# Optimization experiments

Measured on AMD Instinct MI355X. Metric: run time of the kernel, lower is better.

## Reference

```python
import jax, jax.numpy as jnp
import numpy as np
import math

B, T = 2, 1024
D, H, L = 1024, 16, 2
DH = D // H          # 64
R = DH // 2          # 32 rotation blocks
AV, OV = 1024, 16384
FF = 4 * D


def _ln(x, g, b, eps=1e-5):
    m = jnp.mean(x, axis=-1, keepdims=True)
    v = jnp.var(x, axis=-1, keepdims=True)
    return (x - m) * jax.lax.rsqrt(v + eps) * g + b


def build_block_diag_rotations(delta):
    # delta: (B,T,R) angles -> (B,T,2R,2R) block-diagonal 2x2 rotations
    c, s = jnp.cos(delta), jnp.sin(delta)
    Bd, Td, Rd = delta.shape
    M = jnp.zeros((Bd, Td, 2 * Rd, 2 * Rd), dtype=delta.dtype)
    i = 2 * jnp.arange(Rd)
    M = M.at[..., i, i].set(c)
    M = M.at[..., i + 1, i + 1].set(c)
    M = M.at[..., i, i + 1].set(-s)
    M = M.at[..., i + 1, i].set(s)
    return M


def parallel_prefix_product(M):
    # cumulative matrix product along seq axis (associative scan)
    return jax.lax.associative_scan(jnp.matmul, M, axis=1)


def setup_inputs() -> dict:
    key = jax.random.key(0)
    ks = jax.random.split(key, 32)
    std = 0.02
    p = {
        "actions": jax.random.randint(ks[0], (B, T), 0, AV),
        "observations": jax.random.randint(ks[1], (B, T), 0, OV),
        "action_emb": jax.random.normal(ks[2], (AV, D), jnp.float32) * std,
        "obs_emb": jax.random.normal(ks[3], (OV, D), jnp.float32) * std,
        "lie_w": jax.random.normal(ks[4], (D, R), jnp.float32) * std,
        "lie_b": jnp.zeros((R,), jnp.float32),
        "Wq": jax.random.normal(ks[5], (L, D, D), jnp.float32) * std,
        "bq": jnp.zeros((L, D), jnp.float32),
        "Wk": jax.random.normal(ks[6], (L, D, D), jnp.float32) * std,
        "bk": jnp.zeros((L, D), jnp.float32),
        "Wv": jax.random.normal(ks[7], (L, D, D), jnp.float32) * std,
        "bv": jnp.zeros((L, D), jnp.float32),
        "Wo": jax.random.normal(ks[8], (L, D, D), jnp.float32) * std,
        "bo": jnp.zeros((L, D), jnp.float32),
        "ln1_g": jnp.ones((L, D), jnp.float32),
        "ln1_b": jnp.zeros((L, D), jnp.float32),
        "ln2_g": jnp.ones((L, D), jnp.float32),
        "ln2_b": jnp.zeros((L, D), jnp.float32),
        "w1": jax.random.normal(ks[9], (L, D, FF), jnp.float32) * std,
        "b1": jnp.zeros((L, FF), jnp.float32),
        "w2": jax.random.normal(ks[10], (L, FF, D), jnp.float32) * std,
        "b2": jnp.zeros((L, D), jnp.float32),
        "out_g": jnp.ones((D,), jnp.float32),
        "out_bln": jnp.zeros((D,), jnp.float32),
        "out_w": jax.random.normal(ks[11], (D, OV), jnp.float32) * std,
        "out_b": jnp.zeros((OV,), jnp.float32),
    }
    return p


def reference(actions, observations, action_emb, obs_emb, lie_w, lie_b,
              Wq, bq, Wk, bk, Wv, bv, Wo, bo,
              ln1_g, ln1_b, ln2_g, ln2_b, w1, b1, w2, b2,
              out_g, out_bln, out_w, out_b):
    # position state: action embeddings -> Lie algebra -> SO(d_head) prefix products
    a_emb = action_emb[actions]                      # (B,T,D)
    delta = a_emb @ lie_w + lie_b                    # (B,T,R)
    M = build_block_diag_rotations(delta)            # (B,T,DH,DH)
    P = parallel_prefix_product(M)                   # (B,T,DH,DH)

    x = obs_emb[observations]                        # (B,T,D)
    causal = jnp.triu(jnp.ones((T, T), dtype=bool), k=1)
    scale = math.sqrt(DH)

    for l in range(L):
        h = _ln(x, ln1_g[l], ln1_b[l])
        Q = (h @ Wq[l] + bq[l]).reshape(B, T, H, DH)
        K = (h @ Wk[l] + bk[l]).reshape(B, T, H, DH)
        V = (h @ Wv[l] + bv[l]).reshape(B, T, H, DH)
        # generalized RoPE: rotate every head by the cumulative matrix P_t
        Qr = jnp.einsum('btij,bthj->bthi', P, Q)
        Kr = jnp.einsum('btij,bthj->bthi', P, K)
        scores = jnp.einsum('bthd,bshd->bhts', Qr, Kr) / scale
        scores = jnp.where(causal, -jnp.inf, scores)
        attn = jax.nn.softmax(scores, axis=-1)
        o = jnp.einsum('bhts,bshd->bthd', attn, V).reshape(B, T, D)
        x = x + (o @ Wo[l] + bo[l])
        h2 = _ln(x, ln2_g[l], ln2_b[l])
        x = x + (jax.nn.gelu(h2 @ w1[l] + b1[l], approximate=False) @ w2[l] + b2[l])

    x = _ln(x, out_g, out_bln)
    return x @ out_w + out_b                         # (B,T,OV)
```

## Files before the change

### kernel.cpp

```cpp
#include <hip/hip_runtime.h>
#include <cstdint>
#include <cstddef>


using u16 = unsigned short;
using u32 = unsigned int;

typedef __bf16 bf16x8 __attribute__((ext_vector_type(8)));
typedef float  f32x4  __attribute__((ext_vector_type(4)));

__device__ __forceinline__ u16 f2bf(float f) {
  union { float f; u32 u; } v; v.f = f;
  u32 r = v.u + 0x7fffu + ((v.u >> 16) & 1u);
  return (u16)(r >> 16);
}
__device__ __forceinline__ float bf2f(u16 u) {
  union { u32 u; float f; } v; v.u = ((u32)u) << 16;
  return v.f;
}

__device__ __forceinline__ void gll16(const void* g, void* l) {
  __builtin_amdgcn_global_load_lds((__attribute__((address_space(1))) void*)(g),
                                   (__attribute__((address_space(3))) void*)(l),
                                   16, 0, 0);
}

__global__ __launch_bounds__(256) void transpose_f2b(
    const float* __restrict__ in, u16* __restrict__ out, int K, int N)
{
  __shared__ float tile[64][65];
  const int n0 = blockIdx.x * 64, k0 = blockIdx.y * 64;
  const int tid = threadIdx.x;
  const int rr = tid >> 4, cc = (tid & 15) * 4;
  #pragma unroll
  for (int p = 0; p < 4; ++p) {
    int kk = rr + p * 16;
    float4 v = *(const float4*)(in + (size_t)(k0 + kk) * N + n0 + cc);
    tile[kk][cc] = v.x; tile[kk][cc + 1] = v.y;
    tile[kk][cc + 2] = v.z; tile[kk][cc + 3] = v.w;
  }
  __syncthreads();
  #pragma unroll
  for (int p = 0; p < 4; ++p) {
    int nn = rr + p * 16;
    u32 lo = (u32)f2bf(tile[cc + 0][nn]) | ((u32)f2bf(tile[cc + 1][nn]) << 16);
    u32 hi = (u32)f2bf(tile[cc + 2][nn]) | ((u32)f2bf(tile[cc + 3][nn]) << 16);
    uint2 pk; pk.x = lo; pk.y = hi;
    *(uint2*)(out + (size_t)(n0 + nn) * K + k0 + cc) = pk;
  }
}

__global__ __launch_bounds__(256) void fuse_bias(
    const float* __restrict__ bq, const float* __restrict__ bk,
    const float* __restrict__ bv, float* __restrict__ out)
{
  int idx = blockIdx.x * 256 + threadIdx.x;
  int l = idx / 3072, r = idx % 3072;
  const float* src = (r < 1024) ? bq : ((r < 2048) ? bk : bv);
  out[idx] = src[l * 1024 + (r & 1023)];
}

__global__ __launch_bounds__(256) void delta_kernel(
    const int* __restrict__ actions, const float* __restrict__ aemb,
    const float* __restrict__ lie_w, const float* __restrict__ lie_b,
    float* __restrict__ delta)
{
  const int bt = blockIdx.x;
  const int a = actions[bt];
  const float* e = aemb + (size_t)a * 1024;
  const int r = threadIdx.x >> 3, part = threadIdx.x & 7;
  float s = 0.f;
  const int j0 = part * 128;
  for (int j = j0; j < j0 + 128; ++j)
    s += e[j] * lie_w[(size_t)j * 32 + r];
  s += __shfl_xor(s, 1); s += __shfl_xor(s, 2); s += __shfl_xor(s, 4);
  if (part == 0) delta[(size_t)bt * 32 + r] = s + lie_b[r];
}

__global__ __launch_bounds__(256) void scan_theta(
    const float* __restrict__ delta, float2* __restrict__ cs)
{
  const int b = blockIdx.x >> 5, r = blockIdx.x & 31;
  const int tid = threadIdx.x;
  float d0[4];
  #pragma unroll
  for (int i = 0; i < 4; ++i)
    d0[i] = delta[((size_t)b * 1024 + tid * 4 + i) * 32 + r];
  d0[1] += d0[0]; d0[2] += d0[1]; d0[3] += d0[2];
  __shared__ float sc[256];
  sc[tid] = d0[3];
  __syncthreads();
  for (int off = 1; off < 256; off <<= 1) {
    float v = (tid >= off) ? sc[tid - off] : 0.f;
    __syncthreads();
    sc[tid] += v;
    __syncthreads();
  }
  float ex = sc[tid] - d0[3];
  #pragma unroll
  for (int i = 0; i < 4; ++i) {
    float th = ex + d0[i];
    float2 v; v.x = cosf(th); v.y = sinf(th);
    cs[((size_t)b * 1024 + tid * 4 + i) * 32 + r] = v;
  }
}

__global__ __launch_bounds__(256) void gather_x(
    const int* __restrict__ obs, const float* __restrict__ emb,
    float* __restrict__ x)
{
  const int idx = blockIdx.x * 256 + threadIdx.x;
  const int bt = idx >> 8, c = idx & 255;
  *(float4*)(x + (size_t)bt * 1024 + c * 4) =
      *(const float4*)(emb + (size_t)obs[bt] * 1024 + c * 4);
}

__global__ __launch_bounds__(256) void ln_bf16(
    const float* __restrict__ x, const float* __restrict__ g,
    const float* __restrict__ bb, u16* __restrict__ out)
{
  const int row = blockIdx.x, tid = threadIdx.x;
  const float4 v = *(const float4*)(x + (size_t)row * 1024 + tid * 4);
  float s = v.x + v.y + v.z + v.w;
  float q = v.x * v.x + v.y * v.y + v.z * v.z + v.w * v.w;
  #pragma unroll
  for (int off = 32; off; off >>= 1) { s += __shfl_xor(s, off); q += __shfl_xor(q, off); }
  __shared__ float red[8];
  const int wid = tid >> 6, lane = tid & 63;
  if (lane == 0) { red[wid] = s; red[4 + wid] = q; }
  __syncthreads();
  s = red[0] + red[1] + red[2] + red[3];
  q = red[4] + red[5] + red[6] + red[7];
  const float mean = s * (1.f / 1024.f);
  const float var = q * (1.f / 1024.f) - mean * mean;
  const float rstd = rsqrtf(var + 1e-5f);
  float a0 = (v.x - mean) * rstd * g[tid * 4 + 0] + bb[tid * 4 + 0];
  float a1 = (v.y - mean) * rstd * g[tid * 4 + 1] + bb[tid * 4 + 1];
  float a2 = (v.z - mean) * rstd * g[tid * 4 + 2] + bb[tid * 4 + 2];
  float a3 = (v.w - mean) * rstd * g[tid * 4 + 3] + bb[tid * 4 + 3];
  uint2 pk;
  pk.x = (u32)f2bf(a0) | ((u32)f2bf(a1) << 16);
  pk.y = (u32)f2bf(a2) | ((u32)f2bf(a3) << 16);
  *(uint2*)(out + (size_t)row * 1024 + tid * 4) = pk;
}

template<int MODE>
__global__ __launch_bounds__(256) void gemm_bt(
    const u16* __restrict__ A, const u16* __restrict__ Bt,
    const float* __restrict__ bias, const float* res, void* outp,
    const float2* __restrict__ cs, int N, int K, int ypx)
{
  __shared__ u16 As[128 * 32];
  __shared__ u16 Bs[128 * 32];
  const int id = blockIdx.x;
  const int loc = id >> 3;
  const int bx = loc & 15;
  const int by = (id & 7) * ypx + (loc >> 4);
  const int tid = threadIdx.x;
  const int lane = tid & 63, wid = tid >> 6;
  const int wm = wid & 1, wn = wid >> 1;
  const int quad = lane >> 4, lq = lane & 15;
  const int m0 = bx * 128, n0 = by * 128;

  f32x4 acc[4][4] = {};
  const int nkb = K >> 5;
  for (int kb = 0; kb < nkb; ++kb) {
    __syncthreads();
    const int kof = kb * 32;
    #pragma unroll
    for (int rep = 0; rep < 2; ++rep) {
      int c = rep * 256 + tid;
      int row = c >> 2, kc = (c & 3) * 8;
      gll16(A + (size_t)(m0 + row) * K + kof + kc, As + c * 8);
      gll16(Bt + (size_t)(n0 + row) * K + kof + kc, Bs + c * 8);
    }
    __syncthreads();
    bf16x8 a[4], b[4];
    #pragma unroll
    for (int i = 0; i < 4; ++i)
      a[i] = *(const bf16x8*)(As + (wm * 64 + i * 16 + lq) * 32 + quad * 8);
    #pragma unroll
    for (int j = 0; j < 4; ++j)
      b[j] = *(const bf16x8*)(Bs + (wn * 64 + j * 16 + lq) * 32 + quad * 8);
    #pragma unroll
    for (int i = 0; i < 4; ++i)
      #pragma unroll
      for (int j = 0; j < 4; ++j)
        acc[i][j] = __builtin_amdgcn_mfma_f32_16x16x32_bf16(a[i], b[j], acc[i][j], 0, 0, 0);
  }

  #pragma unroll
  for (int i = 0; i < 4; ++i) {
    const int gm0 = m0 + wm * 64 + i * 16 + quad * 4;
    #pragma unroll
    for (int j = 0; j < 4; ++j) {
      const int gn = n0 + wn * 64 + j * 16 + lq;
      const float bv = bias[gn];
      f32x4 v = acc[i][j];
      if constexpr (MODE == 0) {
        u16* O = (u16*)outp;
        #pragma unroll
        for (int r = 0; r < 4; ++r) O[(size_t)(gm0 + r) * N + gn] = f2bf(v[r] + bv);
      } else if constexpr (MODE == 1) {
        float* O = (float*)outp;
        #pragma unroll
        for (int r = 0; r < 4; ++r) {
          size_t idx = (size_t)(gm0 + r) * N + gn;
          O[idx] = res[idx] + v[r] + bv;
        }
      } else if constexpr (MODE == 2) {
        u16* O = (u16*)outp;
        #pragma unroll
        for (int r = 0; r < 4; ++r) {
          float t = v[r] + bv;
          O[(size_t)(gm0 + r) * N + gn] =
              f2bf(0.5f * t * (1.f + erff(t * 0.70710678118654752f)));
        }
      } else if constexpr (MODE == 3) {
        float* O = (float*)outp;
        #pragma unroll
        for (int r = 0; r < 4; ++r) O[(size_t)(gm0 + r) * N + gn] = v[r] + bv;
      } else {
        u16* Qb = (u16*)outp;
        u16* Kb = Qb + (size_t)2048 * 1024;
        u16* Vtb = Kb + (size_t)2048 * 1024;
        const int region = gn >> 10;
        if (region < 2) {
          u16* O = region ? Kb : Qb;
          const int dcol = gn & 1023;
          const int rb = (gn & 63) >> 1;
          const bool odd = (gn & 1) != 0;
          #pragma unroll
          for (int r = 0; r < 4; ++r) {
            float val = v[r] + bv;
            float part = __shfl_xor(val, 1);
            float2 c = cs[(size_t)(gm0 + r) * 32 + rb];
            float rot = odd ? (c.y * part + c.x * val)
                            : (c.x * val - c.y * part);
            O[(size_t)(gm0 + r) * 1024 + dcol] = f2bf(rot);
          }
        } else {
          const int gn2 = gn - 2048;
          const int b = gm0 >> 10, t = gm0 & 1023;
          u32 lo = (u32)f2bf(v[0] + bv) | ((u32)f2bf(v[1] + bv) << 16);
          u32 hi = (u32)f2bf(v[2] + bv) | ((u32)f2bf(v[3] + bv) << 16);
          uint2 pk; pk.x = lo; pk.y = hi;
          size_t idx = ((size_t)(b * 16 + (gn2 >> 6)) * 64 + (gn2 & 63)) * 1024 + t;
          *(uint2*)(Vtb + idx) = pk;
        }
      }
    }
  }
}

__global__ __launch_bounds__(256) void attn_kernel(
    const u16* __restrict__ Q, const u16* __restrict__ K,
    const u16* __restrict__ Vt, u16* __restrict__ O)
{
  __shared__ u16 Qs[64 * 80];
  __shared__ u16 Ks[64 * 80];
  __shared__ u16 Vs[64 * 80];
  __shared__ u16 Ps[64 * 80];

  const int tid = threadIdx.x;
  const int lane = tid & 63, wq = tid >> 6;
  const int quad = lane >> 4, lq = lane & 15;
  const int qt = blockIdx.x;
  const int bh = blockIdx.y;
  const int b = bh >> 4, h = bh & 15;

  const size_t qbase = (size_t)b * 1024 * 1024 + (size_t)qt * 64 * 1024 + h * 64;
  #pragma unroll
  for (int rep = 0; rep < 3; ++rep) {
    int c = rep * 256 + tid;
    if (c < 640) {
      int row = c / 10, rr = c % 10; if (rr >= 8) rr = 0;
      gll16(Q + qbase + (size_t)row * 1024 + rr * 8, Qs + c * 8);
    }
  }

  f32x4 o_acc[4] = {};
  float m_run[4], l_run[4];
  #pragma unroll
  for (int r = 0; r < 4; ++r) { m_run[r] = -1e30f; l_run[r] = 0.f; }

  for (int kt = 0; kt <= qt; ++kt) {
    __syncthreads();
    const size_t kbase = (size_t)b * 1024 * 1024 + (size_t)kt * 64 * 1024 + h * 64;
    const size_t vbase = (size_t)bh * 64 * 1024 + kt * 64;
    #pragma unroll
    for (int rep = 0; rep < 3; ++rep) {
      int c = rep * 256 + tid;
      if (c < 640) {
        int row = c / 10, rr = c % 10; if (rr >= 8) rr = 0;
        gll16(K + kbase + (size_t)row * 1024 + rr * 8, Ks + c * 8);
        gll16(Vt + vbase + (size_t)row * 1024 + rr * 8, Vs + c * 8);
      }
    }
    __syncthreads();

    f32x4 s[4] = {};
    #pragma unroll
    for (int ks = 0; ks < 2; ++ks) {
      bf16x8 aq = *(const bf16x8*)(Qs + (wq * 16 + lq) * 80 + ks * 32 + quad * 8);
      #pragma unroll
      for (int j = 0; j < 4; ++j) {
        bf16x8 bk = *(const bf16x8*)(Ks + (j * 16 + lq) * 80 + ks * 32 + quad * 8);
        s[j] = __builtin_amdgcn_mfma_f32_16x16x32_bf16(aq, bk, s[j], 0, 0, 0);
      }
    }

    float mt[4] = {-1e30f, -1e30f, -1e30f, -1e30f};
    const int qr0 = qt * 64 + wq * 16 + quad * 4;
    const bool diag = (kt == qt);
    #pragma unroll
    for (int j = 0; j < 4; ++j) {
      const int kp = kt * 64 + j * 16 + lq;
      #pragma unroll
      for (int r = 0; r < 4; ++r) {
        float v = s[j][r] * 0.125f;
        if (diag && kp > qr0 + r) v = -1e30f;
        s[j][r] = v;
        mt[r] = fmaxf(mt[r], v);
      }
    }
    #pragma unroll
    for (int r = 0; r < 4; ++r)
      #pragma unroll
      for (int off = 1; off < 16; off <<= 1)
        mt[r] = fmaxf(mt[r], __shfl_xor(mt[r], off));

    float alpha[4], rs[4];
    #pragma unroll
    for (int r = 0; r < 4; ++r) {
      float mn = fmaxf(m_run[r], mt[r]);
      alpha[r] = __expf(m_run[r] - mn);
      m_run[r] = mn;
      rs[r] = 0.f;
    }
    #pragma unroll
    for (int j = 0; j < 4; ++j)
      #pragma unroll
      for (int r = 0; r < 4; ++r) {
        float p = __expf(s[j][r] - m_run[r]);
        s[j][r] = p;
        rs[r] += p;
      }
    #pragma unroll
    for (int r = 0; r < 4; ++r) {
      #pragma unroll
      for (int off = 1; off < 16; off <<= 1)
        rs[r] += __shfl_xor(rs[r], off);
      l_run[r] = l_run[r] * alpha[r] + rs[r];
      o_acc[0][r] *= alpha[r]; o_acc[1][r] *= alpha[r];
      o_acc[2][r] *= alpha[r]; o_acc[3][r] *= alpha[r];
    }

    #pragma unroll
    for (int j = 0; j < 4; ++j)
      #pragma unroll
      for (int r = 0; r < 4; ++r)
        Ps[(wq * 16 + quad * 4 + r) * 80 + j * 16 + lq] = f2bf(s[j][r]);
    asm volatile("s_waitcnt lgkmcnt(0)" ::: "memory");

    #pragma unroll
    for (int ks = 0; ks < 2; ++ks) {
      bf16x8 ap = *(const bf16x8*)(Ps + (wq * 16 + lq) * 80 + ks * 32 + quad * 8);
      #pragma unroll
      for (int jd = 0; jd < 4; ++jd) {
        bf16x8 bv = *(const bf16x8*)(Vs + (jd * 16 + lq) * 80 + ks * 32 + quad * 8);
        o_acc[jd] = __builtin_amdgcn_mfma_f32_16x16x32_bf16(ap, bv, o_acc[jd], 0, 0, 0);
      }
    }
  }

  #pragma unroll
  for (int r = 0; r < 4; ++r) {
    const int t = qt * 64 + wq * 16 + quad * 4 + r;
    const float inv = 1.f / l_run[r];
    const size_t base = ((size_t)(b * 1024 + t) * 16 + h) * 64;
    #pragma unroll
    for (int jd = 0; jd < 4; ++jd)
      O[base + jd * 16 + lq] = f2bf(o_acc[jd][r] * inv);
  }
}

extern "C" void kernel_launch(void* const* d_in, const int* in_sizes, int n_in,
                              void* d_out, int out_size, void* d_ws, size_t ws_size,
                              hipStream_t stream) {
  const int*   actions      = (const int*)d_in[0];
  const int*   observations = (const int*)d_in[1];
  const float* action_emb   = (const float*)d_in[2];
  const float* obs_emb      = (const float*)d_in[3];
  const float* lie_w        = (const float*)d_in[4];
  const float* lie_b        = (const float*)d_in[5];
  const float* Wq = (const float*)d_in[6];  const float* bq = (const float*)d_in[7];
  const float* Wk = (const float*)d_in[8];  const float* bk = (const float*)d_in[9];
  const float* Wv = (const float*)d_in[10]; const float* bvp = (const float*)d_in[11];
  const float* Wo = (const float*)d_in[12]; const float* bo = (const float*)d_in[13];
  const float* ln1_g = (const float*)d_in[14]; const float* ln1_b = (const float*)d_in[15];
  const float* ln2_g = (const float*)d_in[16]; const float* ln2_b = (const float*)d_in[17];
  const float* w1 = (const float*)d_in[18]; const float* b1 = (const float*)d_in[19];
  const float* w2 = (const float*)d_in[20]; const float* b2 = (const float*)d_in[21];
  const float* out_g = (const float*)d_in[22]; const float* out_bln = (const float*)d_in[23];
  const float* out_w = (const float*)d_in[24]; const float* out_b = (const float*)d_in[25];
  float* out = (float*)d_out;

  char* basep = (char*)d_ws;
  size_t off = 0;
  auto take = [&](size_t bytes) -> char* {
    char* p = basep + off;
    off += (bytes + 255) & ~(size_t)255;
    return p;
  };
  u16* qkvT = (u16*)take((size_t)2 * 3072 * 1024 * 2);
  u16* woT  = (u16*)take((size_t)2 * 1024 * 1024 * 2);
  u16* w1T  = (u16*)take((size_t)2 * 4096 * 1024 * 2);
  u16* w2T  = (u16*)take((size_t)2 * 4096 * 1024 * 2);
  u16* owT  = (u16*)take((size_t)16384 * 1024 * 2);
  float* biasf = (float*)take((size_t)2 * 3072 * 4);
  float*  xbuf  = (float*)take((size_t)2048 * 1024 * 4);
  u16*    hbuf  = (u16*)take((size_t)2048 * 1024 * 2);
  u16*    qkvb  = (u16*)take((size_t)3 * 2048 * 1024 * 2);
  u16*    qbuf  = qkvb;
  u16*    kbuf  = qkvb + (size_t)2048 * 1024;
  u16*    vtg   = qkvb + (size_t)2 * 2048 * 1024;
  u16*    obuf  = (u16*)take((size_t)2048 * 1024 * 2);
  u16*    ubuf  = (u16*)take((size_t)2048 * 4096 * 2);
  float*  dbuf  = (float*)take((size_t)2048 * 32 * 4);
  float2* csbuf = (float2*)take((size_t)2048 * 32 * 8);

  for (int l = 0; l < 2; ++l) {
    size_t mo = (size_t)l * 1024 * 1024;
    size_t qo = (size_t)l * 3072 * 1024;
    size_t fo = (size_t)l * 4096 * 1024;
    transpose_f2b<<<dim3(16, 16), 256, 0, stream>>>(Wq + mo, qkvT + qo, 1024, 1024);
    transpose_f2b<<<dim3(16, 16), 256, 0, stream>>>(Wk + mo, qkvT + qo + (size_t)1024 * 1024, 1024, 1024);
    transpose_f2b<<<dim3(16, 16), 256, 0, stream>>>(Wv + mo, qkvT + qo + (size_t)2048 * 1024, 1024, 1024);
    transpose_f2b<<<dim3(16, 16), 256, 0, stream>>>(Wo + mo, woT + mo, 1024, 1024);
    transpose_f2b<<<dim3(64, 16), 256, 0, stream>>>(w1 + fo, w1T + fo, 1024, 4096);
    transpose_f2b<<<dim3(16, 64), 256, 0, stream>>>(w2 + fo, w2T + fo, 4096, 1024);
  }
  transpose_f2b<<<dim3(256, 16), 256, 0, stream>>>(out_w, owT, 1024, 16384);
  fuse_bias<<<24, 256, 0, stream>>>(bq, bk, bvp, biasf);

  delta_kernel<<<2048, 256, 0, stream>>>(actions, action_emb, lie_w, lie_b, dbuf);
  scan_theta<<<64, 256, 0, stream>>>(dbuf, csbuf);
  gather_x<<<2048, 256, 0, stream>>>(observations, obs_emb, xbuf);

  for (int l = 0; l < 2; ++l) {
    size_t mo = (size_t)l * 1024 * 1024;
    size_t qo = (size_t)l * 3072 * 1024;
    size_t fo = (size_t)l * 4096 * 1024;
    ln_bf16<<<2048, 256, 0, stream>>>(xbuf, ln1_g + l * 1024, ln1_b + l * 1024, hbuf);
    gemm_bt<5><<<16 * 24, 256, 0, stream>>>(hbuf, qkvT + qo, biasf + l * 3072, nullptr,
                                            qkvb, csbuf, 3072, 1024, 3);
    attn_kernel<<<dim3(16, 32), 256, 0, stream>>>(qbuf, kbuf, vtg, obuf);
    gemm_bt<1><<<16 * 8, 256, 0, stream>>>(obuf, woT + mo, bo + l * 1024, xbuf,
                                           xbuf, nullptr, 1024, 1024, 1);
    ln_bf16<<<2048, 256, 0, stream>>>(xbuf, ln2_g + l * 1024, ln2_b + l * 1024, hbuf);
    gemm_bt<2><<<16 * 32, 256, 0, stream>>>(hbuf, w1T + fo, b1 + l * 4096, nullptr,
                                            ubuf, nullptr, 4096, 1024, 4);
    gemm_bt<1><<<16 * 8, 256, 0, stream>>>(ubuf, w2T + fo, b2 + l * 1024, xbuf,
                                           xbuf, nullptr, 1024, 4096, 1);
  }
  ln_bf16<<<2048, 256, 0, stream>>>(xbuf, out_g, out_bln, hbuf);
  gemm_bt<3><<<16 * 128, 256, 0, stream>>>(hbuf, owT, out_b, nullptr,
                                           out, nullptr, 16384, 1024, 16);
}
```

Before: 1.108 ms.

## Split-K the N=1024 GEMMs and fuse residual reduction into LayerNorm

The Wo and W2 projections, which only have 128 output tiles, now run split-K (2 and 4 ways). Each split writes fp32 partial sums, and a new ln_red kernel adds them to the residual with the bias and then applies the next LayerNorm in the same pass. This fills more CUs on the small-N GEMMs and removes the separate residual-epilogue and LN launches. The weight transposes are also batched into fewer launches using grid z, and the GEMM grid swizzle is replaced by a plain 2D grid. The cost is extra fp32 partial traffic, with partW reusing ubuf, and a possible loss of L2 locality from dropping the swizzle.

Result: faster. 912.9 us (-17.6%).

```diff
diff --git a/kernel.cpp b/kernel.cpp
--- a/kernel.cpp
+++ b/kernel.cpp
@@ -14,10 +14,6 @@
   u32 r = v.u + 0x7fffu + ((v.u >> 16) & 1u);
   return (u16)(r >> 16);
 }
-__device__ __forceinline__ float bf2f(u16 u) {
-  union { u32 u; float f; } v; v.u = ((u32)u) << 16;
-  return v.f;
-}
 
 __device__ __forceinline__ void gll16(const void* g, void* l) {
   __builtin_amdgcn_global_load_lds((__attribute__((address_space(1))) void*)(g),
@@ -26,8 +22,10 @@
 }
 
 __global__ __launch_bounds__(256) void transpose_f2b(
-    const float* __restrict__ in, u16* __restrict__ out, int K, int N)
-{
+    const float* __restrict__ in0, u16* __restrict__ out0, int K, int N)
+{
+  const float* in = in0 + (size_t)blockIdx.z * K * N;
+  u16* out = out0 + (size_t)blockIdx.z * K * N;
   __shared__ float tile[64][65];
   const int n0 = blockIdx.x * 64, k0 = blockIdx.y * 64;
   const int tid = threadIdx.x;
@@ -43,10 +41,37 @@
   #pragma unroll
   for (int p = 0; p < 4; ++p) {
     int nn = rr + p * 16;
-    u32 lo = (u32)f2bf(tile[cc + 0][nn]) | ((u32)f2bf(tile[cc + 1][nn]) << 16);
-    u32 hi = (u32)f2bf(tile[cc + 2][nn]) | ((u32)f2bf(tile[cc + 3][nn]) << 16);
-    uint2 pk; pk.x = lo; pk.y = hi;
+    uint2 pk;
+    pk.x = (u32)f2bf(tile[cc + 0][nn]) | ((u32)f2bf(tile[cc + 1][nn]) << 16);
+    pk.y = (u32)f2bf(tile[cc + 2][nn]) | ((u32)f2bf(tile[cc + 3][nn]) << 16);
     *(uint2*)(out + (size_t)(n0 + nn) * K + k0 + cc) = pk;
+  }
+}
+
+struct TP8 { const float* s[8]; u16* d[8]; };
+__global__ __launch_bounds__(256) void transpose8(TP8 p)
+{
+  const float* in = p.s[blockIdx.z];
+  u16* out = p.d[blockIdx.z];
+  __shared__ float tile[64][65];
+  const int n0 = blockIdx.x * 64, k0 = blockIdx.y * 64;
+  const int tid = threadIdx.x;
+  const int rr = tid >> 4, cc = (tid & 15) * 4;
+  #pragma unroll
+  for (int p2 = 0; p2 < 4; ++p2) {
+    int kk = rr + p2 * 16;
+    float4 v = *(const float4*)(in + (size_t)(k0 + kk) * 1024 + n0 + cc);
+    tile[kk][cc] = v.x; tile[kk][cc + 1] = v.y;
+    tile[kk][cc + 2] = v.z; tile[kk][cc + 3] = v.w;
+  }
+  __syncthreads();
+  #pragma unroll
+  for (int p2 = 0; p2 < 4; ++p2) {
+    int nn = rr + p2 * 16;
+    uint2 pk;
+    pk.x = (u32)f2bf(tile[cc + 0][nn]) | ((u32)f2bf(tile[cc + 1][nn]) << 16);
+    pk.y = (u32)f2bf(tile[cc + 2][nn]) | ((u32)f2bf(tile[cc + 3][nn]) << 16);
+    *(uint2*)(out + (size_t)(n0 + nn) * 1024 + k0 + cc) = pk;
   }
 }
 
@@ -144,35 +169,70 @@
   *(uint2*)(out + (size_t)row * 1024 + tid * 4) = pk;
 }
 
+__global__ __launch_bounds__(256) void ln_red(
+    float* __restrict__ x, const float* __restrict__ part, int sk,
+    const float* __restrict__ bias, const float* __restrict__ g,
+    const float* __restrict__ bb, u16* __restrict__ out)
+{
+  const int row = blockIdx.x, tid = threadIdx.x;
+  const size_t base = (size_t)row * 1024 + tid * 4;
+  float4 v = *(const float4*)(x + base);
+  const float4 bia = *(const float4*)(bias + tid * 4);
+  v.x += bia.x; v.y += bia.y; v.z += bia.z; v.w += bia.w;
+  for (int sp = 0; sp < sk; ++sp) {
+    float4 pv = *(const float4*)(part + (size_t)sp * 2048 * 1024 + base);
+    v.x += pv.x; v.y += pv.y; v.z += pv.z; v.w += pv.w;
+  }
+  *(float4*)(x + base) = v;
+  float s = v.x + v.y + v.z + v.w;
+  float q = v.x * v.x + v.y * v.y + v.z * v.z + v.w * v.w;
+  #pragma unroll
+  for (int off = 32; off; off >>= 1) { s += __shfl_xor(s, off); q += __shfl_xor(q, off); }
+  __shared__ float red[8];
+  const int wid = tid >> 6, lane = tid & 63;
+  if (lane == 0) { red[wid] = s; red[4 + wid] = q; }
+  __syncthreads();
+  s = red[0] + red[1] + red[2] + red[3];
+  q = red[4] + red[5] + red[6] + red[7];
+  const float mean = s * (1.f / 1024.f);
+  const float var = q * (1.f / 1024.f) - mean * mean;
+  const float rstd = rsqrtf(var + 1e-5f);
+  float a0 = (v.x - mean) * rstd * g[tid * 4 + 0] + bb[tid * 4 + 0];
+  float a1 = (v.y - mean) * rstd * g[tid * 4 + 1] + bb[tid * 4 + 1];
+  float a2 = (v.z - mean) * rstd * g[tid * 4 + 2] + bb[tid * 4 + 2];
+  float a3 = (v.w - mean) * rstd * g[tid * 4 + 3] + bb[tid * 4 + 3];
+  uint2 pk;
+  pk.x = (u32)f2bf(a0) | ((u32)f2bf(a1) << 16);
+  pk.y = (u32)f2bf(a2) | ((u32)f2bf(a3) << 16);
+  *(uint2*)(out + base) = pk;
+}
+
 template<int MODE>
 __global__ __launch_bounds__(256) void gemm_bt(
     const u16* __restrict__ A, const u16* __restrict__ Bt,
-    const float* __restrict__ bias, const float* res, void* outp,
-    const float2* __restrict__ cs, int N, int K, int ypx)
+    const float* __restrict__ bias, void* outp,
+    const float2* __restrict__ cs, int N, int Kc, int ldk)
 {
   __shared__ u16 As[128 * 32];
   __shared__ u16 Bs[128 * 32];
-  const int id = blockIdx.x;
-  const int loc = id >> 3;
-  const int bx = loc & 15;
-  const int by = (id & 7) * ypx + (loc >> 4);
   const int tid = threadIdx.x;
   const int lane = tid & 63, wid = tid >> 6;
   const int wm = wid & 1, wn = wid >> 1;
   const int quad = lane >> 4, lq = lane & 15;
-  const int m0 = bx * 128, n0 = by * 128;
+  const int m0 = blockIdx.x * 128, n0 = blockIdx.y * 128;
+  const int koff = blockIdx.z * Kc;
 
   f32x4 acc[4][4] = {};
-  const int nkb = K >> 5;
+  const int nkb = Kc >> 5;
   for (int kb = 0; kb < nkb; ++kb) {
     __syncthreads();
-    const int kof = kb * 32;
+    const int kof = koff + kb * 32;
     #pragma unroll
     for (int rep = 0; rep < 2; ++rep) {
       int c = rep * 256 + tid;
       int row = c >> 2, kc = (c & 3) * 8;
-      gll16(A + (size_t)(m0 + row) * K + kof + kc, As + c * 8);
-      gll16(Bt + (size_t)(n0 + row) * K + kof + kc, Bs + c * 8);
+      gll16(A + (size_t)(m0 + row) * ldk + kof + kc, As + c * 8);
+      gll16(Bt + (size_t)(n0 + row) * ldk + kof + kc, Bs + c * 8);
     }
     __syncthreads();
     bf16x8 a[4], b[4];
@@ -195,20 +255,14 @@
     #pragma unroll
     for (int j = 0; j < 4; ++j) {
       const int gn = n0 + wn * 64 + j * 16 + lq;
-      const float bv = bias[gn];
       f32x4 v = acc[i][j];
       if constexpr (MODE == 0) {
+        const float bv = bias[gn];
         u16* O = (u16*)outp;
         #pragma unroll
         for (int r = 0; r < 4; ++r) O[(size_t)(gm0 + r) * N + gn] = f2bf(v[r] + bv);
-      } else if constexpr (MODE == 1) {
-        float* O = (float*)outp;
-        #pragma unroll
-        for (int r = 0; r < 4; ++r) {
-          size_t idx = (size_t)(gm0 + r) * N + gn;
-          O[idx] = res[idx] + v[r] + bv;
-        }
       } else if constexpr (MODE == 2) {
+        const float bv = bias[gn];
         u16* O = (u16*)outp;
         #pragma unroll
         for (int r = 0; r < 4; ++r) {
@@ -217,10 +271,16 @@
               f2bf(0.5f * t * (1.f + erff(t * 0.70710678118654752f)));
         }
       } else if constexpr (MODE == 3) {
+        const float bv = bias[gn];
         float* O = (float*)outp;
         #pragma unroll
         for (int r = 0; r < 4; ++r) O[(size_t)(gm0 + r) * N + gn] = v[r] + bv;
+      } else if constexpr (MODE == 6) {
+        float* O = (float*)outp + (size_t)blockIdx.z * 2048 * N;
+        #pragma unroll
+        for (int r = 0; r < 4; ++r) O[(size_t)(gm0 + r) * N + gn] = v[r];
       } else {
+        const float bv = bias[gn];
         u16* Qb = (u16*)outp;
         u16* Kb = Qb + (size_t)2048 * 1024;
         u16* Vtb = Kb + (size_t)2048 * 1024;
@@ -242,9 +302,9 @@
         } else {
           const int gn2 = gn - 2048;
           const int b = gm0 >> 10, t = gm0 & 1023;
-          u32 lo = (u32)f2bf(v[0] + bv) | ((u32)f2bf(v[1] + bv) << 16);
-          u32 hi = (u32)f2bf(v[2] + bv) | ((u32)f2bf(v[3] + bv) << 16);
-          uint2 pk; pk.x = lo; pk.y = hi;
+          uint2 pk;
+          pk.x = (u32)f2bf(v[0] + bv) | ((u32)f2bf(v[1] + bv) << 16);
+          pk.y = (u32)f2bf(v[2] + bv) | ((u32)f2bf(v[3] + bv) << 16);
           size_t idx = ((size_t)(b * 16 + (gn2 >> 6)) * 64 + (gn2 & 63)) * 1024 + t;
           *(uint2*)(Vtb + idx) = pk;
         }
@@ -427,44 +487,50 @@
   u16*    vtg   = qkvb + (size_t)2 * 2048 * 1024;
   u16*    obuf  = (u16*)take((size_t)2048 * 1024 * 2);
   u16*    ubuf  = (u16*)take((size_t)2048 * 4096 * 2);
+  float*  partW = (float*)ubuf;
+  float*  partF = (float*)take((size_t)4 * 2048 * 1024 * 4);
   float*  dbuf  = (float*)take((size_t)2048 * 32 * 4);
   float2* csbuf = (float2*)take((size_t)2048 * 32 * 8);
 
+  TP8 tp;
+  for (int l = 0; l < 2; ++l) {
+    size_t mo = (size_t)l * 1024 * 1024;
+    size_t qo = (size_t)l * 3072 * 1024;
+    tp.s[l * 4 + 0] = Wq + mo; tp.d[l * 4 + 0] = qkvT + qo;
+    tp.s[l * 4 + 1] = Wk + mo; tp.d[l * 4 + 1] = qkvT + qo + (size_t)1024 * 1024;
+    tp.s[l * 4 + 2] = Wv + mo; tp.d[l * 4 + 2] = qkvT + qo + (size_t)2048 * 1024;
+    tp.s[l * 4 + 3] = Wo + mo; tp.d[l * 4 + 3] = woT + mo;
+  }
+  transpose8<<<dim3(16, 16, 8), 256, 0, stream>>>(tp);
+  transpose_f2b<<<dim3(64, 16, 2), 256, 0, stream>>>(w1, w1T, 1024, 4096);
+  transpose_f2b<<<dim3(16, 64, 2), 256, 0, stream>>>(w2, w2T, 4096, 1024);
+  transpose_f2b<<<dim3(256, 16, 1), 256, 0, stream>>>(out_w, owT, 1024, 16384);
+  fuse_bias<<<24, 256, 0, stream>>>(bq, bk, bvp, biasf);
+
+  delta_kernel<<<2048, 256, 0, stream>>>(actions, action_emb, lie_w, lie_b, dbuf);
+  scan_theta<<<64, 256, 0, stream>>>(dbuf, csbuf);
+  gather_x<<<2048, 256, 0, stream>>>(observations, obs_emb, xbuf);
+
+  ln_bf16<<<2048, 256, 0, stream>>>(xbuf, ln1_g, ln1_b, hbuf);
   for (int l = 0; l < 2; ++l) {
     size_t mo = (size_t)l * 1024 * 1024;
     size_t qo = (size_t)l * 3072 * 1024;
     size_t fo = (size_t)l * 4096 * 1024;
-    transpose_f2b<<<dim3(16, 16), 256, 0, stream>>>(Wq + mo, qkvT + qo, 1024, 1024);
-    transpose_f2b<<<dim3(16, 16), 256, 0, stream>>>(Wk + mo, qkvT + qo + (size_t)1024 * 1024, 1024, 1024);
-    transpose_f2b<<<dim3(16, 16), 256, 0, stream>>>(Wv + mo, qkvT + qo + (size_t)2048 * 1024, 1024, 1024);
-    transpose_f2b<<<dim3(16, 16), 256, 0, stream>>>(Wo + mo, woT + mo, 1024, 1024);
-    transpose_f2b<<<dim3(64, 16), 256, 0, stream>>>(w1 + fo, w1T + fo, 1024, 4096);
-    transpose_f2b<<<dim3(16, 64), 256, 0, stream>>>(w2 + fo, w2T + fo, 4096, 1024);
-  }
-  transpose_f2b<<<dim3(256, 16), 256, 0, stream>>>(out_w, owT, 1024, 16384);
-  fuse_bias<<<24, 256, 0, stream>>>(bq, bk, bvp, biasf);
-
-  delta_kernel<<<2048, 256, 0, stream>>>(actions, action_emb, lie_w, lie_b, dbuf);
-  scan_theta<<<64, 256, 0, stream>>>(dbuf, csbuf);
-  gather_x<<<2048, 256, 0, stream>>>(observations, obs_emb, xbuf);
-
-  for (int l = 0; l < 2; ++l) {
-    size_t mo = (size_t)l * 1024 * 1024;
-    size_t qo = (size_t)l * 3072 * 1024;
-    size_t fo = (size_t)l * 4096 * 1024;
-    ln_bf16<<<2048, 256, 0, stream>>>(xbuf, ln1_g + l * 1024, ln1_b + l * 1024, hbuf);
-    gemm_bt<5><<<16 * 24, 256, 0, stream>>>(hbuf, qkvT + qo, biasf + l * 3072, nullptr,
-                                            qkvb, csbuf, 3072, 1024, 3);
+    gemm_bt<5><<<dim3(16, 24, 1), 256, 0, stream>>>(hbuf, qkvT + qo, biasf + l * 3072,
+                                                    qkvb, csbuf, 3072, 1024, 1024);
     attn_kernel<<<dim3(16, 32), 256, 0, stream>>>(qbuf, kbuf, vtg, obuf);
-    gemm_bt<1><<<16 * 8, 256, 0, stream>>>(obuf, woT + mo, bo + l * 1024, xbuf,
-                                           xbuf, nullptr, 1024, 1024, 1);
-    ln_bf16<<<2048, 256, 0, stream>>>(xbuf, ln2_g + l * 1024, ln2_b + l * 1024, hbuf);
-    gemm_bt<2><<<16 * 32, 256, 0, stream>>>(hbuf, w1T + fo, b1 + l * 4096, nullptr,
-                                            ubuf, nullptr, 4096, 1024, 4);
-    gemm_bt<1><<<16 * 8, 256, 0, stream>>>(ubuf, w2T + fo, b2 + l * 1024, xbuf,
-                                           xbuf, nullptr, 1024, 4096, 1);
-  }
-  ln_bf16<<<2048, 256, 0, stream>>>(xbuf, out_g, out_bln, hbuf);
-  gemm_bt<3><<<16 * 128, 256, 0, stream>>>(hbuf, owT, out_b, nullptr,
-                                           out, nullptr, 16384, 1024, 16);
-}
+    gemm_bt<6><<<dim3(16, 8, 2), 256, 0, stream>>>(obuf, woT + mo, nullptr,
+                                                   partW, nullptr, 1024, 512, 1024);
+    ln_red<<<2048, 256, 0, stream>>>(xbuf, partW, 2, bo + l * 1024,
+                                     ln2_g + l * 1024, ln2_b + l * 1024, hbuf);
+    gemm_bt<2><<<dim3(16, 32, 1), 256, 0, stream>>>(hbuf, w1T + fo, b1 + l * 4096,
+                                                    ubuf, nullptr, 4096, 1024, 1024);
+    gemm_bt<6><<<dim3(16, 8, 4), 256, 0, stream>>>(ubuf, w2T + fo, nullptr,
+                                                   partF, nullptr, 1024, 1024, 4096);
+    const float* ng = (l == 0) ? (ln1_g + 1024) : out_g;
+    const float* nb = (l == 0) ? (ln1_b + 1024) : out_bln;
+    ln_red<<<2048, 256, 0, stream>>>(xbuf, partF, 4, b2 + l * 1024, ng, nb, hbuf);
+  }
+  gemm_bt<3><<<dim3(16, 128, 1), 256, 0, stream>>>(hbuf, owT, out_b,
+                                                   out, nullptr, 16384, 1024, 1024);
+}
```
